# Performance work log

Hardware: AMD Instinct MI355X
Metric: run time of the kernel (lower is better)

## Reference

```python
import jax, jax.numpy as jnp
import numpy as np

TOP_K = 2
TEMP = 0.9
EPS = 1e-5
B, S, D, F, E = 2, 2048, 1024, 4096, 8


def setup_inputs() -> dict:
    key = jax.random.key(0)
    ks = jax.random.split(key, 4)
    scale_in = 1.0 / np.sqrt(D)
    scale_ff = 1.0 / np.sqrt(F)
    return {
        "x": jax.random.normal(ks[0], (B, S, D), jnp.float32),
        "gate_w": jax.random.normal(ks[1], (D, E), jnp.float32) * scale_in,
        "gate_b": jnp.zeros((E,), jnp.float32),
        "w1": jax.random.normal(ks[2], (E, D, F), jnp.float32) * scale_in,
        "b1": jnp.zeros((E, F), jnp.float32),
        "w2": jax.random.normal(ks[3], (E, F, D), jnp.float32) * scale_ff,
        "b2": jnp.zeros((E, D), jnp.float32),
        "ln_g": jnp.ones((D,), jnp.float32),
        "ln_b": jnp.zeros((D,), jnp.float32),
    }


def _moe_forward(x, gate_w, gate_b, w1, b1, w2, b2, ln_g, ln_b):
    # Gating: top-k masked softmax over experts
    logits = (x @ gate_w + gate_b) / TEMP                       # [B,S,E]
    topk_vals, topk_idx = jax.lax.top_k(logits, TOP_K)          # [B,S,K]
    keep = jax.nn.one_hot(topk_idx, E, dtype=jnp.bool_).any(-2)  # [B,S,E]
    masked = jnp.where(keep, logits, -jnp.inf)
    gate_probs = jax.nn.softmax(masked, axis=-1)                # [B,S,E]

    # Dense all-expert FFN (faithful to the naive original)
    h = jnp.einsum('bsd,edf->bsef', x, w1) + b1                 # [B,S,E,F]
    h = jax.nn.gelu(h, approximate=False)
    expert_out = jnp.einsum('bsef,efd->bsed', h, w2) + b2       # [B,S,E,D]

    out = jnp.einsum('bse,bsed->bsd', gate_probs, expert_out)   # combine

    # Post LayerNorm (dropout is identity in eval)
    mu = out.mean(-1, keepdims=True)
    var = out.var(-1, keepdims=True)
    out = (out - mu) / jnp.sqrt(var + EPS) * ln_g + ln_b
    return out


def reference(x, gate_w, gate_b, w1, b1, w2, b2, ln_g, ln_b):
    return _moe_forward(x, gate_w, gate_b, w1, b1, w2, b2, ln_g, ln_b)
```

## Files before the change

kernel.cpp:

```cpp
#include <hip/hip_runtime.h>
#include <stdint.h>
#include <stddef.h>

#define T_TOK 4096
#define DD    1024
#define FF    4096
#define EE    8
#define MAXROWS 9216
#define MAXTILES 72

typedef unsigned short u16;
typedef unsigned int   u32;
typedef short  sh8 __attribute__((ext_vector_type(8)));
typedef __bf16 bf8 __attribute__((ext_vector_type(8)));
typedef float  fl4 __attribute__((ext_vector_type(4)));

__device__ __forceinline__ u32 f2b_u(float f){
  u32 u = __float_as_uint(f);
  return (u + 0x7FFFu + ((u >> 16) & 1u)) >> 16;
}
__device__ __forceinline__ u16 f2b(float f){ return (u16)f2b_u(f); }
__device__ __forceinline__ u32 pack2(float a, float b){ return f2b_u(a) | (f2b_u(b) << 16); }

__device__ __forceinline__ void gl_lds16(const u16* g, u16* l){
  __builtin_amdgcn_global_load_lds(
      (const __attribute__((address_space(1))) u32*)(g),
      (__attribute__((address_space(3))) u32*)(l), 16, 0, 0);
}

__device__ __forceinline__ fl4 mfma16(sh8 a, sh8 b, fl4 c){
  return __builtin_amdgcn_mfma_f32_16x16x32_bf16(
      __builtin_bit_cast(bf8, a), __builtin_bit_cast(bf8, b), c, 0, 0, 0);
}

__global__ __launch_bounds__(256) void k_cvt_x(const float* __restrict__ x,
                                               u16* __restrict__ xb){
  size_t i = ((size_t)blockIdx.x * 256 + threadIdx.x) * 8;
  float4 a = *(const float4*)(x + i);
  float4 b = *(const float4*)(x + i + 4);
  uint4 v;
  v.x = pack2(a.x, a.y); v.y = pack2(a.z, a.w);
  v.z = pack2(b.x, b.y); v.w = pack2(b.z, b.w);
  *(uint4*)(xb + i) = v;
}

__global__ __launch_bounds__(256) void k_gate(const float* __restrict__ x,
    const float* __restrict__ gw, const float* __restrict__ gb,
    int* __restrict__ tidx, float* __restrict__ tp, int* __restrict__ meta){
  int lane = threadIdx.x & 63;
  int t = blockIdx.x * 4 + (threadIdx.x >> 6);
  const float* xr = x + (size_t)t * DD;
  float a0=0,a1=0,a2=0,a3=0,a4=0,a5=0,a6=0,a7=0;
  #pragma unroll
  for (int i = 0; i < 16; i++){
    int d = i * 64 + lane;
    float xv = xr[d];
    const float4* g4 = (const float4*)(gw + (size_t)d * EE);
    float4 p = g4[0], q = g4[1];
    a0 += xv*p.x; a1 += xv*p.y; a2 += xv*p.z; a3 += xv*p.w;
    a4 += xv*q.x; a5 += xv*q.y; a6 += xv*q.z; a7 += xv*q.w;
  }
  #pragma unroll
  for (int off = 32; off > 0; off >>= 1){
    a0 += __shfl_xor(a0, off, 64); a1 += __shfl_xor(a1, off, 64);
    a2 += __shfl_xor(a2, off, 64); a3 += __shfl_xor(a3, off, 64);
    a4 += __shfl_xor(a4, off, 64); a5 += __shfl_xor(a5, off, 64);
    a6 += __shfl_xor(a6, off, 64); a7 += __shfl_xor(a7, off, 64);
  }
  if (lane == 0){
    float l[8] = {a0,a1,a2,a3,a4,a5,a6,a7};
    #pragma unroll
    for (int e = 0; e < 8; e++) l[e] = (l[e] + gb[e]) * (1.0f / 0.9f);
    int i1 = 0;
    #pragma unroll
    for (int e = 1; e < 8; e++) if (l[e] > l[i1]) i1 = e;
    int i2 = (i1 == 0) ? 1 : 0;
    #pragma unroll
    for (int e = 0; e < 8; e++) if (e != i1 && l[e] > l[i2]) i2 = e;
    float ex = expf(l[i2] - l[i1]);
    float inv = 1.0f / (1.0f + ex);
    tidx[2*t] = i1; tidx[2*t+1] = i2;
    tp[2*t] = inv;  tp[2*t+1] = ex * inv;
    atomicAdd(&meta[i1], 1);
    atomicAdd(&meta[i2], 1);
  }
}

__global__ void k_scan(int* __restrict__ meta){
  if (threadIdx.x == 0){
    int rowbase = 0, total = 0;
    for (int e = 0; e < EE; e++){
      int c = meta[e];
      meta[16 + e] = rowbase;
      int nt = (c + 127) >> 7;
      for (int i = 0; i < nt; i++){
        meta[32 + total]  = e;
        meta[104 + total] = rowbase + i * 128;
        total++;
      }
      rowbase += nt << 7;
    }
    meta[24] = total;
  }
}

__global__ __launch_bounds__(256) void k_fill(const int* __restrict__ tidx,
    const float* __restrict__ tp, int* __restrict__ meta,
    int* __restrict__ rowmap, float* __restrict__ rowp){
  int t = blockIdx.x * 256 + threadIdx.x;
  if (t >= T_TOK) return;
  #pragma unroll
  for (int k = 0; k < 2; k++){
    int e = tidx[2*t + k];
    int pos = atomicAdd(&meta[8 + e], 1);
    int row = meta[16 + e] + pos;
    rowmap[row] = (t << 1) | k;
    rowp[row] = tp[2*t + k];
  }
}

__global__ __launch_bounds__(256) void k_cvtw(const float* __restrict__ src,
    u16* __restrict__ dst, int R, int C){
  __shared__ float tile[64][65];
  int e = blockIdx.z;
  const float* se = src + (size_t)e * R * C;
  u16* de = dst + (size_t)e * R * C;
  int rblk = blockIdx.y * 64, cblk = blockIdx.x * 64;
  int tid = threadIdx.x;
  int lr = tid >> 4, lc = tid & 15;
  #pragma unroll
  for (int i = 0; i < 4; i++){
    int row = lr + i * 16;
    float4 v = *(const float4*)(se + (size_t)(rblk + row) * C + cblk + lc * 4);
    tile[row][lc*4+0] = v.x; tile[row][lc*4+1] = v.y;
    tile[row][lc*4+2] = v.z; tile[row][lc*4+3] = v.w;
  }
  __syncthreads();
  int c = tid >> 2, seg = tid & 3;
  u32 o[8];
  #pragma unroll
  for (int j = 0; j < 8; j++){
    float f0 = tile[seg*16 + 2*j    ][c];
    float f1 = tile[seg*16 + 2*j + 1][c];
    o[j] = pack2(f0, f1);
  }
  u16* dp = de + (size_t)(cblk + c) * R + rblk + seg * 16;
  *(uint4*)(dp)     = make_uint4(o[0], o[1], o[2], o[3]);
  *(uint4*)(dp + 8) = make_uint4(o[4], o[5], o[6], o[7]);
}

__global__ __launch_bounds__(256) void k_gemm_h(
    const u16* __restrict__ Xb, const u16* __restrict__ Wt,
    const float* __restrict__ b1, const int* __restrict__ meta,
    const int* __restrict__ rowmap, u16* __restrict__ H){
  __shared__ u16 As[128 * 32];
  __shared__ u16 Bs[128 * 32];
  int tx = blockIdx.x;
  if (tx >= meta[24]) return;
  int e = meta[32 + tx], row0 = meta[104 + tx];
  int n0 = blockIdx.y * 128;
  int tid = threadIdx.x;
  int ra = tid >> 2, seg = tid & 3;
  int t0 = rowmap[row0 + ra] >> 1;       if (t0 < 0) t0 = 0;
  int t1 = rowmap[row0 + 64 + ra] >> 1;  if (t1 < 0) t1 = 0;
  const u16* gA0 = Xb + (size_t)t0 * DD + seg * 8;
  const u16* gA1 = Xb + (size_t)t1 * DD + seg * 8;
  const u16* Be  = Wt + ((size_t)e * FF + n0) * DD;
  const u16* gB0 = Be + (size_t)ra * DD + seg * 8;
  const u16* gB1 = Be + (size_t)(ra + 64) * DD + seg * 8;
  u16* lA0 = As + tid * 8; u16* lA1 = As + 2048 + tid * 8;
  u16* lB0 = Bs + tid * 8; u16* lB1 = Bs + 2048 + tid * 8;

  int lane = tid & 63, wv = tid >> 6;
  int wm = wv & 1, wn = wv >> 1;
  int lr = lane & 15, lq = lane >> 4;
  const u16* pA = As + (wm * 64 + lr) * 32 + lq * 8;
  const u16* pB = Bs + (wn * 64 + lr) * 32 + lq * 8;

  fl4 acc[4][4];
  #pragma unroll
  for (int mi = 0; mi < 4; mi++)
    #pragma unroll
    for (int ni = 0; ni < 4; ni++) acc[mi][ni] = (fl4){0.f,0.f,0.f,0.f};

  for (int k0 = 0; k0 < DD; k0 += 32){
    gl_lds16(gA0 + k0, lA0);
    gl_lds16(gA1 + k0, lA1);
    gl_lds16(gB0 + k0, lB0);
    gl_lds16(gB1 + k0, lB1);
    __syncthreads();
    sh8 a[4], b[4];
    #pragma unroll
    for (int mi = 0; mi < 4; mi++) a[mi] = *(const sh8*)(pA + mi * 16 * 32);
    #pragma unroll
    for (int ni = 0; ni < 4; ni++) b[ni] = *(const sh8*)(pB + ni * 16 * 32);
    #pragma unroll
    for (int mi = 0; mi < 4; mi++)
      #pragma unroll
      for (int ni = 0; ni < 4; ni++)
        acc[mi][ni] = mfma16(a[mi], b[ni], acc[mi][ni]);
    __syncthreads();
  }

  const float* b1e = b1 + (size_t)e * FF;
  float bias[4];
  #pragma unroll
  for (int ni = 0; ni < 4; ni++) bias[ni] = b1e[n0 + wn*64 + ni*16 + lr];
  #pragma unroll
  for (int mi = 0; mi < 4; mi++){
    int grb = row0 + wm * 64 + mi * 16 + lq * 4;
    #pragma unroll
    for (int ni = 0; ni < 4; ni++){
      int gc = n0 + wn * 64 + ni * 16 + lr;
      #pragma unroll
      for (int r = 0; r < 4; r++){
        float v = acc[mi][ni][r] + bias[ni];
        v = 0.5f * v * (1.0f + erff(v * 0.70710678118654752f));
        H[(size_t)(grb + r) * FF + gc] = f2b(v);
      }
    }
  }
}

__global__ __launch_bounds__(256) void k_gemm_y(
    const u16* __restrict__ H, const u16* __restrict__ Wt,
    const float* __restrict__ b2, const int* __restrict__ meta,
    const int* __restrict__ rowmap, const float* __restrict__ rowp,
    float* __restrict__ slots){
  __shared__ u16 As[128 * 32];
  __shared__ u16 Bs[128 * 32];
  int tx = blockIdx.x;
  if (tx >= meta[24]) return;
  int e = meta[32 + tx], row0 = meta[104 + tx];
  int n0 = blockIdx.y * 128;
  int tid = threadIdx.x;
  int ra = tid >> 2, seg = tid & 3;
  const u16* gA0 = H + (size_t)(row0 + ra) * FF + seg * 8;
  const u16* gA1 = H + (size_t)(row0 + 64 + ra) * FF + seg * 8;
  const u16* Be  = Wt + ((size_t)e * DD + n0) * FF;
  const u16* gB0 = Be + (size_t)ra * FF + seg * 8;
  const u16* gB1 = Be + (size_t)(ra + 64) * FF + seg * 8;
  u16* lA0 = As + tid * 8; u16* lA1 = As + 2048 + tid * 8;
  u16* lB0 = Bs + tid * 8; u16* lB1 = Bs + 2048 + tid * 8;

  int lane = tid & 63, wv = tid >> 6;
  int wm = wv & 1, wn = wv >> 1;
  int lr = lane & 15, lq = lane >> 4;
  const u16* pA = As + (wm * 64 + lr) * 32 + lq * 8;
  const u16* pB = Bs + (wn * 64 + lr) * 32 + lq * 8;

  fl4 acc[4][4];
  #pragma unroll
  for (int mi = 0; mi < 4; mi++)
    #pragma unroll
    for (int ni = 0; ni < 4; ni++) acc[mi][ni] = (fl4){0.f,0.f,0.f,0.f};

  for (int k0 = 0; k0 < FF; k0 += 32){
    gl_lds16(gA0 + k0, lA0);
    gl_lds16(gA1 + k0, lA1);
    gl_lds16(gB0 + k0, lB0);
    gl_lds16(gB1 + k0, lB1);
    __syncthreads();
    sh8 a[4], b[4];
    #pragma unroll
    for (int mi = 0; mi < 4; mi++) a[mi] = *(const sh8*)(pA + mi * 16 * 32);
    #pragma unroll
    for (int ni = 0; ni < 4; ni++) b[ni] = *(const sh8*)(pB + ni * 16 * 32);
    #pragma unroll
    for (int mi = 0; mi < 4; mi++)
      #pragma unroll
      for (int ni = 0; ni < 4; ni++)
        acc[mi][ni] = mfma16(a[mi], b[ni], acc[mi][ni]);
    __syncthreads();
  }

  const float* b2e = b2 + (size_t)e * DD;
  float bias[4];
  #pragma unroll
  for (int ni = 0; ni < 4; ni++) bias[ni] = b2e[n0 + wn*64 + ni*16 + lr];
  #pragma unroll
  for (int mi = 0; mi < 4; mi++){
    int grb = row0 + wm * 64 + mi * 16 + lq * 4;
    #pragma unroll
    for (int r = 0; r < 4; r++){
      int gr = grb + r;
      int sl = rowmap[gr];
      if (sl < 0) continue;
      float p = rowp[gr];
      #pragma unroll
      for (int ni = 0; ni < 4; ni++){
        int gc = n0 + wn * 64 + ni * 16 + lr;
        slots[(size_t)sl * DD + gc] = (acc[mi][ni][r] + bias[ni]) * p;
      }
    }
  }
}

__global__ __launch_bounds__(256) void k_ln(const float* __restrict__ slots,
    const float* __restrict__ lng, const float* __restrict__ lnb,
    float* __restrict__ out){
  int lane = threadIdx.x & 63;
  int t = blockIdx.x * 4 + (threadIdx.x >> 6);
  const float* s0 = slots + (size_t)(2 * t) * DD;
  const float* s1 = s0 + DD;
  float y[16];
  float sum = 0.f, sq = 0.f;
  #pragma unroll
  for (int i = 0; i < 2; i++){
    int d = lane * 8 + i * 512;
    float4 p0 = *(const float4*)(s0 + d);
    float4 p1 = *(const float4*)(s0 + d + 4);
    float4 q0 = *(const float4*)(s1 + d);
    float4 q1 = *(const float4*)(s1 + d + 4);
    y[i*8+0]=p0.x+q0.x; y[i*8+1]=p0.y+q0.y; y[i*8+2]=p0.z+q0.z; y[i*8+3]=p0.w+q0.w;
    y[i*8+4]=p1.x+q1.x; y[i*8+5]=p1.y+q1.y; y[i*8+6]=p1.z+q1.z; y[i*8+7]=p1.w+q1.w;
  }
  #pragma unroll
  for (int j = 0; j < 16; j++){ sum += y[j]; sq += y[j]*y[j]; }
  #pragma unroll
  for (int off = 32; off > 0; off >>= 1){
    sum += __shfl_xor(sum, off, 64);
    sq  += __shfl_xor(sq,  off, 64);
  }
  float mu = sum * (1.0f / DD);
  float var = sq * (1.0f / DD) - mu * mu;
  float rs = 1.0f / sqrtf(var + 1e-5f);
  #pragma unroll
  for (int i = 0; i < 2; i++){
    int d = lane * 8 + i * 512;
    float4 g0 = *(const float4*)(lng + d), g1 = *(const float4*)(lng + d + 4);
    float4 c0 = *(const float4*)(lnb + d), c1 = *(const float4*)(lnb + d + 4);
    float4 o0, o1;
    o0.x=(y[i*8+0]-mu)*rs*g0.x+c0.x; o0.y=(y[i*8+1]-mu)*rs*g0.y+c0.y;
    o0.z=(y[i*8+2]-mu)*rs*g0.z+c0.z; o0.w=(y[i*8+3]-mu)*rs*g0.w+c0.w;
    o1.x=(y[i*8+4]-mu)*rs*g1.x+c1.x; o1.y=(y[i*8+5]-mu)*rs*g1.y+c1.y;
    o1.z=(y[i*8+6]-mu)*rs*g1.z+c1.z; o1.w=(y[i*8+7]-mu)*rs*g1.w+c1.w;
    *(float4*)(out + (size_t)t * DD + d)     = o0;
    *(float4*)(out + (size_t)t * DD + d + 4) = o1;
  }
}

extern "C" void kernel_launch(void* const* d_in, const int* in_sizes, int n_in,
                              void* d_out, int out_size, void* d_ws, size_t ws_size,
                              hipStream_t stream){
  const float* x   = (const float*)d_in[0];
  const float* gw  = (const float*)d_in[1];
  const float* gb  = (const float*)d_in[2];
  const float* w1  = (const float*)d_in[3];
  const float* b1  = (const float*)d_in[4];
  const float* w2  = (const float*)d_in[5];
  const float* b2  = (const float*)d_in[6];
  const float* lng = (const float*)d_in[7];
  const float* lnb = (const float*)d_in[8];
  float* out = (float*)d_out;

  char* ws = (char*)d_ws;
  size_t off = 0;
  auto alloc = [&](size_t bytes) -> void* {
    void* p = ws + off;
    off = (off + bytes + 255) & ~(size_t)255;
    return p;
  };
  int*   meta   = (int*)  alloc(256 * 4);
  int*   rowmap = (int*)  alloc(MAXROWS * 4);
  float* rowp   = (float*)alloc(MAXROWS * 4);
  int*   tidx   = (int*)  alloc(2 * T_TOK * 4);
  float* tp     = (float*)alloc(2 * T_TOK * 4);
  u16*   Xb     = (u16*)  alloc((size_t)T_TOK * DD * 2);
  float* slots  = (float*)alloc((size_t)T_TOK * 2 * DD * 4);
  u16*   H      = (u16*)  alloc((size_t)MAXROWS * FF * 2);
  u16*   Wt     = (u16*)  alloc((size_t)EE * DD * FF * 2);
  (void)ws_size; (void)in_sizes; (void)n_in; (void)out_size;

  hipMemsetAsync(meta, 0, 64, stream);
  hipMemsetAsync(rowmap, 0xFF, MAXROWS * 4, stream);

  k_cvt_x<<<(T_TOK * DD) / (256 * 8), 256, 0, stream>>>(x, Xb);
  k_gate <<<T_TOK / 4, 256, 0, stream>>>(x, gw, gb, tidx, tp, meta);
  k_scan <<<1, 64, 0, stream>>>(meta);
  k_fill <<<T_TOK / 256, 256, 0, stream>>>(tidx, tp, meta, rowmap, rowp);

  k_cvtw <<<dim3(FF / 64, DD / 64, EE), 256, 0, stream>>>(w1, Wt, DD, FF);
  k_gemm_h<<<dim3(MAXTILES, FF / 128), 256, 0, stream>>>(Xb, Wt, b1, meta, rowmap, H);
  k_cvtw <<<dim3(DD / 64, FF / 64, EE), 256, 0, stream>>>(w2, Wt, FF, DD);
  k_gemm_y<<<dim3(MAXTILES, DD / 128), 256, 0, stream>>>(H, Wt, b2, meta, rowmap, rowp, slots);

  k_ln   <<<T_TOK / 4, 256, 0, stream>>>(slots, lng, lnb, out);
}
```

Before: 727.9 us.

## Deepen GEMM K-tile to 64 with XOR-swizzled LDS, tanh GELU, fused scan/fill

Both expert GEMMs now stage a K-depth of 64 per iteration instead of 32, which halves the number of barrier pairs per tile. The shared-memory layout gets an XOR swizzle to avoid bank conflicts on the wider rows. The exact erf GELU is replaced with a sigmoid-based tanh approximation using a fast exp and reciprocal. The scan and fill kernels are merged into one single-block kernel that uses shared-memory atomics. The GELU change alters numerics slightly, and the single-block fill serialises the routing over 256 threads.

New measurement: 709.8 us. 1.03x faster.

```diff
diff --git a/kernel.cpp b/kernel.cpp
--- a/kernel.cpp
+++ b/kernel.cpp
@@ -31,6 +31,14 @@
 __device__ __forceinline__ fl4 mfma16(sh8 a, sh8 b, fl4 c){
   return __builtin_amdgcn_mfma_f32_16x16x32_bf16(
       __builtin_bit_cast(bf8, a), __builtin_bit_cast(bf8, b), c, 0, 0, 0);
+}
+
+__device__ __forceinline__ float gelu_f(float x){
+  float x2 = x * x;
+  float t  = fmaf(0.07135481283f, x2, 1.5957691216f);
+  float u  = x * t;
+  float e  = __expf(-u);
+  return x * __frcp_rn(1.0f + e);
 }
 
 __global__ __launch_bounds__(256) void k_cvt_x(const float* __restrict__ x,
@@ -86,12 +94,18 @@
   }
 }
 
-__global__ void k_scan(int* __restrict__ meta){
-  if (threadIdx.x == 0){
+__global__ __launch_bounds__(256) void k_fillscan(const int* __restrict__ tidx,
+    const float* __restrict__ tp, int* __restrict__ meta,
+    int* __restrict__ rowmap, float* __restrict__ rowp){
+  __shared__ int sbase[EE];
+  __shared__ int scur[EE];
+  int tid = threadIdx.x;
+  if (tid < EE) scur[tid] = 0;
+  if (tid == 0){
     int rowbase = 0, total = 0;
     for (int e = 0; e < EE; e++){
       int c = meta[e];
-      meta[16 + e] = rowbase;
+      sbase[e] = rowbase;
       int nt = (c + 127) >> 7;
       for (int i = 0; i < nt; i++){
         meta[32 + total]  = e;
@@ -102,20 +116,16 @@
     }
     meta[24] = total;
   }
-}
-
-__global__ __launch_bounds__(256) void k_fill(const int* __restrict__ tidx,
-    const float* __restrict__ tp, int* __restrict__ meta,
-    int* __restrict__ rowmap, float* __restrict__ rowp){
-  int t = blockIdx.x * 256 + threadIdx.x;
-  if (t >= T_TOK) return;
-  #pragma unroll
-  for (int k = 0; k < 2; k++){
-    int e = tidx[2*t + k];
-    int pos = atomicAdd(&meta[8 + e], 1);
-    int row = meta[16 + e] + pos;
-    rowmap[row] = (t << 1) | k;
-    rowp[row] = tp[2*t + k];
+  __syncthreads();
+  for (int t = tid; t < T_TOK; t += 256){
+    #pragma unroll
+    for (int k = 0; k < 2; k++){
+      int e = tidx[2*t + k];
+      int pos = atomicAdd(&scur[e], 1);
+      int row = sbase[e] + pos;
+      rowmap[row] = (t << 1) | k;
+      rowp[row] = tp[2*t + k];
+    }
   }
 }
 
@@ -153,29 +163,36 @@
     const u16* __restrict__ Xb, const u16* __restrict__ Wt,
     const float* __restrict__ b1, const int* __restrict__ meta,
     const int* __restrict__ rowmap, u16* __restrict__ H){
-  __shared__ u16 As[128 * 32];
-  __shared__ u16 Bs[128 * 32];
+  __shared__ u16 As[128 * 64];
+  __shared__ u16 Bs[128 * 64];
   int tx = blockIdx.x;
   if (tx >= meta[24]) return;
   int e = meta[32 + tx], row0 = meta[104 + tx];
   int n0 = blockIdx.y * 128;
   int tid = threadIdx.x;
-  int ra = tid >> 2, seg = tid & 3;
-  int t0 = rowmap[row0 + ra] >> 1;       if (t0 < 0) t0 = 0;
-  int t1 = rowmap[row0 + 64 + ra] >> 1;  if (t1 < 0) t1 = 0;
-  const u16* gA0 = Xb + (size_t)t0 * DD + seg * 8;
-  const u16* gA1 = Xb + (size_t)t1 * DD + seg * 8;
-  const u16* Be  = Wt + ((size_t)e * FF + n0) * DD;
-  const u16* gB0 = Be + (size_t)ra * DD + seg * 8;
-  const u16* gB1 = Be + (size_t)(ra + 64) * DD + seg * 8;
-  u16* lA0 = As + tid * 8; u16* lA1 = As + 2048 + tid * 8;
-  u16* lB0 = Bs + tid * 8; u16* lB1 = Bs + 2048 + tid * 8;
+  int rsub = tid >> 3;
+  int sw_st = ((tid & 7) ^ (rsub & 7)) * 8;
+  const u16* Be = Wt + ((size_t)e * FF + n0) * DD;
+  const u16* gA[4];
+  const u16* gB[4];
+  #pragma unroll
+  for (int j = 0; j < 4; j++){
+    int row = j * 32 + rsub;
+    int rm = rowmap[row0 + row];
+    int tok = (rm < 0) ? 0 : (rm >> 1);
+    gA[j] = Xb + (size_t)tok * DD + sw_st;
+    gB[j] = Be + (size_t)row * DD + sw_st;
+  }
+  u16* lA = As + tid * 8;
+  u16* lB = Bs + tid * 8;
 
   int lane = tid & 63, wv = tid >> 6;
   int wm = wv & 1, wn = wv >> 1;
   int lr = lane & 15, lq = lane >> 4;
-  const u16* pA = As + (wm * 64 + lr) * 32 + lq * 8;
-  const u16* pB = Bs + (wn * 64 + lr) * 32 + lq * 8;
+  int sw0 = ((lq    ) ^ (lr & 7)) * 8;
+  int sw1 = ((lq + 4) ^ (lr & 7)) * 8;
+  const u16* pA = As + (wm * 64 + lr) * 64;
+  const u16* pB = Bs + (wn * 64 + lr) * 64;
 
   fl4 acc[4][4];
   #pragma unroll
@@ -183,22 +200,27 @@
     #pragma unroll
     for (int ni = 0; ni < 4; ni++) acc[mi][ni] = (fl4){0.f,0.f,0.f,0.f};
 
-  for (int k0 = 0; k0 < DD; k0 += 32){
-    gl_lds16(gA0 + k0, lA0);
-    gl_lds16(gA1 + k0, lA1);
-    gl_lds16(gB0 + k0, lB0);
-    gl_lds16(gB1 + k0, lB1);
+  for (int k0 = 0; k0 < DD; k0 += 64){
+    #pragma unroll
+    for (int j = 0; j < 4; j++){
+      gl_lds16(gA[j] + k0, lA + j * 2048);
+      gl_lds16(gB[j] + k0, lB + j * 2048);
+    }
     __syncthreads();
-    sh8 a[4], b[4];
-    #pragma unroll
-    for (int mi = 0; mi < 4; mi++) a[mi] = *(const sh8*)(pA + mi * 16 * 32);
-    #pragma unroll
-    for (int ni = 0; ni < 4; ni++) b[ni] = *(const sh8*)(pB + ni * 16 * 32);
-    #pragma unroll
-    for (int mi = 0; mi < 4; mi++)
-      #pragma unroll
-      for (int ni = 0; ni < 4; ni++)
-        acc[mi][ni] = mfma16(a[mi], b[ni], acc[mi][ni]);
+    #pragma unroll
+    for (int kk = 0; kk < 2; kk++){
+      int sw = kk ? sw1 : sw0;
+      sh8 a[4], b[4];
+      #pragma unroll
+      for (int mi = 0; mi < 4; mi++) a[mi] = *(const sh8*)(pA + mi * 1024 + sw);
+      #pragma unroll
+      for (int ni = 0; ni < 4; ni++) b[ni] = *(const sh8*)(pB + ni * 1024 + sw);
+      #pragma unroll
+      for (int mi = 0; mi < 4; mi++)
+        #pragma unroll
+        for (int ni = 0; ni < 4; ni++)
+          acc[mi][ni] = mfma16(a[mi], b[ni], acc[mi][ni]);
+    }
     __syncthreads();
   }
 
@@ -215,8 +237,7 @@
       #pragma unroll
       for (int r = 0; r < 4; r++){
         float v = acc[mi][ni][r] + bias[ni];
-        v = 0.5f * v * (1.0f + erff(v * 0.70710678118654752f));
-        H[(size_t)(grb + r) * FF + gc] = f2b(v);
+        H[(size_t)(grb + r) * FF + gc] = f2b(gelu_f(v));
       }
     }
   }
@@ -227,27 +248,34 @@
     const float* __restrict__ b2, const int* __restrict__ meta,
     const int* __restrict__ rowmap, const float* __restrict__ rowp,
     float* __restrict__ slots){
-  __shared__ u16 As[128 * 32];
-  __shared__ u16 Bs[128 * 32];
+  __shared__ u16 As[128 * 64];
+  __shared__ u16 Bs[128 * 64];
   int tx = blockIdx.x;
   if (tx >= meta[24]) return;
   int e = meta[32 + tx], row0 = meta[104 + tx];
   int n0 = blockIdx.y * 128;
   int tid = threadIdx.x;
-  int ra = tid >> 2, seg = tid & 3;
-  const u16* gA0 = H + (size_t)(row0 + ra) * FF + seg * 8;
-  const u16* gA1 = H + (size_t)(row0 + 64 + ra) * FF + seg * 8;
-  const u16* Be  = Wt + ((size_t)e * DD + n0) * FF;
-  const u16* gB0 = Be + (size_t)ra * FF + seg * 8;
-  const u16* gB1 = Be + (size_t)(ra + 64) * FF + seg * 8;
-  u16* lA0 = As + tid * 8; u16* lA1 = As + 2048 + tid * 8;
-  u16* lB0 = Bs + tid * 8; u16* lB1 = Bs + 2048 + tid * 8;
+  int rsub = tid >> 3;
+  int sw_st = ((tid & 7) ^ (rsub & 7)) * 8;
+  const u16* Be = Wt + ((size_t)e * DD + n0) * FF;
+  const u16* gA[4];
+  const u16* gB[4];
+  #pragma unroll
+  for (int j = 0; j < 4; j++){
+    int row = j * 32 + rsub;
+    gA[j] = H + (size_t)(row0 + row) * FF + sw_st;
+    gB[j] = Be + (size_t)row * FF + sw_st;
+  }
+  u16* lA = As + tid * 8;
+  u16* lB = Bs + tid * 8;
 
   int lane = tid & 63, wv = tid >> 6;
   int wm = wv & 1, wn = wv >> 1;
   int lr = lane & 15, lq = lane >> 4;
-  const u16* pA = As + (wm * 64 + lr) * 32 + lq * 8;
-  const u16* pB = Bs + (wn * 64 + lr) * 32 + lq * 8;
+  int sw0 = ((lq    ) ^ (lr & 7)) * 8;
+  int sw1 = ((lq + 4) ^ (lr & 7)) * 8;
+  const u16* pA = As + (wm * 64 + lr) * 64;
+  const u16* pB = Bs + (wn * 64 + lr) * 64;
 
   fl4 acc[4][4];
   #pragma unroll
@@ -255,22 +283,27 @@
     #pragma unroll
     for (int ni = 0; ni < 4; ni++) acc[mi][ni] = (fl4){0.f,0.f,0.f,0.f};
 
-  for (int k0 = 0; k0 < FF; k0 += 32){
-    gl_lds16(gA0 + k0, lA0);
-    gl_lds16(gA1 + k0, lA1);
-    gl_lds16(gB0 + k0, lB0);
-    gl_lds16(gB1 + k0, lB1);
+  for (int k0 = 0; k0 < FF; k0 += 64){
+    #pragma unroll
+    for (int j = 0; j < 4; j++){
+      gl_lds16(gA[j] + k0, lA + j * 2048);
+      gl_lds16(gB[j] + k0, lB + j * 2048);
+    }
     __syncthreads();
-    sh8 a[4], b[4];
-    #pragma unroll
-    for (int mi = 0; mi < 4; mi++) a[mi] = *(const sh8*)(pA + mi * 16 * 32);
-    #pragma unroll
-    for (int ni = 0; ni < 4; ni++) b[ni] = *(const sh8*)(pB + ni * 16 * 32);
-    #pragma unroll
-    for (int mi = 0; mi < 4; mi++)
-      #pragma unroll
-      for (int ni = 0; ni < 4; ni++)
-        acc[mi][ni] = mfma16(a[mi], b[ni], acc[mi][ni]);
+    #pragma unroll
+    for (int kk = 0; kk < 2; kk++){
+      int sw = kk ? sw1 : sw0;
+      sh8 a[4], b[4];
+      #pragma unroll
+      for (int mi = 0; mi < 4; mi++) a[mi] = *(const sh8*)(pA + mi * 1024 + sw);
+      #pragma unroll
+      for (int ni = 0; ni < 4; ni++) b[ni] = *(const sh8*)(pB + ni * 1024 + sw);
+      #pragma unroll
+      for (int mi = 0; mi < 4; mi++)
+        #pragma unroll
+        for (int ni = 0; ni < 4; ni++)
+          acc[mi][ni] = mfma16(a[mi], b[ni], acc[mi][ni]);
+    }
     __syncthreads();
   }
 
@@ -375,15 +408,14 @@
   hipMemsetAsync(meta, 0, 64, stream);
   hipMemsetAsync(rowmap, 0xFF, MAXROWS * 4, stream);
 
-  k_cvt_x<<<(T_TOK * DD) / (256 * 8), 256, 0, stream>>>(x, Xb);
-  k_gate <<<T_TOK / 4, 256, 0, stream>>>(x, gw, gb, tidx, tp, meta);
-  k_scan <<<1, 64, 0, stream>>>(meta);
-  k_fill <<<T_TOK / 256, 256, 0, stream>>>(tidx, tp, meta, rowmap, rowp);
-
-  k_cvtw <<<dim3(FF / 64, DD / 64, EE), 256, 0, stream>>>(w1, Wt, DD, FF);
+  k_cvt_x   <<<(T_TOK * DD) / (256 * 8), 256, 0, stream>>>(x, Xb);
+  k_gate    <<<T_TOK / 4, 256, 0, stream>>>(x, gw, gb, tidx, tp, meta);
+  k_fillscan<<<1, 256, 0, stream>>>(tidx, tp, meta, rowmap, rowp);
+
+  k_cvtw  <<<dim3(FF / 64, DD / 64, EE), 256, 0, stream>>>(w1, Wt, DD, FF);
   k_gemm_h<<<dim3(MAXTILES, FF / 128), 256, 0, stream>>>(Xb, Wt, b1, meta, rowmap, H);
-  k_cvtw <<<dim3(DD / 64, FF / 64, EE), 256, 0, stream>>>(w2, Wt, FF, DD);
+  k_cvtw  <<<dim3(DD / 64, FF / 64, EE), 256, 0, stream>>>(w2, Wt, FF, DD);
   k_gemm_y<<<dim3(MAXTILES, DD / 128), 256, 0, stream>>>(H, Wt, b2, meta, rowmap, rowp, slots);
 
-  k_ln   <<<T_TOK / 4, 256, 0, stream>>>(slots, lng, lnb, out);
-}
+  k_ln    <<<T_TOK / 4, 256, 0, stream>>>(slots, lng, lnb, out);
+}
```
